# Kernel tuning notes

Hardware: AMD Instinct MI355X
Metric: run time of the kernel (lower is better)

Reference implementation:

```python
import jax, jax.numpy as jnp
import numpy as np
import math

B, S, D = 32, 2048, 1024


def setup_inputs() -> dict:
    key = jax.random.key(0)
    ks = jax.random.split(key, 8)
    x = jax.random.normal(ks[0], (B, S, D), dtype=jnp.float32)
    # right-padding mask: True = padding, each row has a random valid length in [S//2, S]
    lengths = jax.random.randint(ks[1], (B, 1), S // 2, S + 1)
    attention_mask = jnp.arange(S)[None, :] >= lengths  # [B, S] bool
    scale = 1.0 / math.sqrt(D)
    gate_w1 = jax.random.normal(ks[2], (D, D // 2), dtype=jnp.float32) * scale
    gate_b1 = jnp.zeros((D // 2,), dtype=jnp.float32)
    gate_w2 = jax.random.normal(ks[3], (D // 2, 1), dtype=jnp.float32) * scale
    gate_b2 = jnp.zeros((1,), dtype=jnp.float32)
    decay_lambda = jnp.float32(0.05)
    attention_query = jax.random.normal(ks[4], (D,), dtype=jnp.float32)
    key_w = jax.random.normal(ks[5], (D, D), dtype=jnp.float32) * scale
    key_b = jnp.zeros((D,), dtype=jnp.float32)
    return {
        "utterance_embeddings": x,
        "attention_mask": attention_mask,
        "gate_w1": gate_w1, "gate_b1": gate_b1,
        "gate_w2": gate_w2, "gate_b2": gate_b2,
        "decay_lambda": decay_lambda,
        "attention_query": attention_query,
        "key_w": key_w, "key_b": key_b,
    }


def reference(utterance_embeddings, attention_mask, gate_w1, gate_b1, gate_w2,
              gate_b2, decay_lambda, attention_query, key_w, key_b):
    x = utterance_embeddings  # [B, S, D]
    bsz, seq_len, dim = x.shape
    # suppression gate: Linear -> GELU(exact) -> Linear -> Sigmoid, output [B, S, 1]
    h = jax.nn.gelu(jnp.einsum('bsd,dk->bsk', x, gate_w1) + gate_b1, approximate=False)
    gate = jax.nn.sigmoid(jnp.einsum('bsk,ko->bso', h, gate_w2) + gate_b2)
    gated = x * gate  # [B, S, D]
    keys = jnp.einsum('bsd,de->bse', gated, key_w) + key_b  # [B, S, D]
    logits = jnp.einsum('d,bsd->bs', attention_query, keys) / jnp.sqrt(jnp.float32(dim))
    t_idx = jnp.arange(seq_len, dtype=jnp.float32)[None, :]  # [1, S]
    valid_lengths = jnp.sum(~attention_mask, axis=1, keepdims=True).astype(jnp.float32)
    penalty_idx = jnp.maximum(valid_lengths - 1.0 - t_idx, 0.0)  # [B, S]
    pos_lambda = jax.nn.softplus(decay_lambda)
    decayed = logits - pos_lambda * penalty_idx
    decayed = jnp.where(attention_mask, jnp.float32(-10000.0), decayed)
    alpha = jax.nn.softmax(decayed, axis=1)  # [B, S]
    scene_vector = jnp.einsum('bs,bsd->bd', alpha, gated)  # [B, D]
    return scene_vector
```

## Files before the change

kernel.cpp:

```cpp
#include <hip/hip_runtime.h>
#include <hip/hip_bf16.h>
#include <math.h>

#define BQ 32
#define SQ 2048
#define DQ 1024
#define NQ 512
#define MQ (BQ*SQ)
#define BM 64
#define BN 512
#define BK 32

typedef __attribute__((ext_vector_type(8))) short bf16x8;
typedef __attribute__((ext_vector_type(4))) short bf16x4;
typedef __attribute__((ext_vector_type(4))) float f32x4;

__device__ __forceinline__ short f2bf(float f){
  return __builtin_bit_cast(short, __float2bfloat16(f));
}

__device__ __forceinline__ void gload_lds16(const void* g, void* l){
  __builtin_amdgcn_global_load_lds(
      (const __attribute__((address_space(1))) unsigned int*)g,
      (__attribute__((address_space(3))) unsigned int*)l, 16, 0, 0);
}

__global__ void k_w1t(const float* __restrict__ w1, short* __restrict__ w1t){
  int i = blockIdx.x*256 + threadIdx.x;
  if (i >= NQ*DQ) return;
  int n = i >> 10, k = i & (DQ-1);
  w1t[i] = f2bf(w1[(size_t)k*NQ + n]);
}

__global__ void k_wq(const float* __restrict__ kw, const float* __restrict__ kb,
                     const float* __restrict__ q, float* __restrict__ wq){
  __shared__ float sh[4];
  int d = blockIdx.x, t = threadIdx.x;
  const float* row = (d < DQ) ? (kw + (size_t)d*DQ) : kb;
  float s = 0.f;
  for (int e=t;e<DQ;e+=256) s += row[e]*q[e];
  #pragma unroll
  for (int o=32;o;o>>=1) s += __shfl_down(s,o);
  if ((t&63)==0) sh[t>>6]=s;
  __syncthreads();
  if (t==0) wq[d] = sh[0]+sh[1]+sh[2]+sh[3];
}

__global__ void k_det(const unsigned int* __restrict__ m, int* __restrict__ flag){
  __shared__ int so, sf;
  int t = threadIdx.x;
  if (t==0){ so=0; sf=0; }
  __syncthreads();
  int o=0, f1=0;
  for (int i=t;i<MQ/4;i+=256){
    unsigned v = m[i];
    if (v==0x3F800000u) f1=1;
    else if (v>1u) o=1;
  }
  if (o) atomicOr(&so,1);
  if (f1) atomicOr(&sf,1);
  __syncthreads();
  if (t==0) *flag = so?2:(sf?1:0);
}

__global__ __launch_bounds__(256) void k_len(const void* __restrict__ maskp,
                                             const int* __restrict__ flag,
                                             int* __restrict__ lens){
  __shared__ int sh[4];
  int b = blockIdx.x, t = threadIdx.x;
  int fl = *flag;
  const unsigned char* m8 = (const unsigned char*)maskp;
  const float* mf = (const float*)maskp;
  const int* mi = (const int*)maskp;
  int cnt = 0;
  #pragma unroll
  for (int i=0;i<8;i++){
    size_t idx = (size_t)b*SQ + t + i*256;
    int mm = (fl==2) ? (m8[idx]!=0) : (fl==1) ? (mf[idx]!=0.0f) : (mi[idx]!=0);
    cnt += mm^1;
  }
  #pragma unroll
  for (int o=32;o;o>>=1) cnt += __shfl_down(cnt,o);
  if ((t&63)==0) sh[t>>6]=cnt;
  __syncthreads();
  if (t==0) lens[b] = sh[0]+sh[1]+sh[2]+sh[3];
}

__global__ __launch_bounds__(512) void k_gate(
    const float* __restrict__ x, const short* __restrict__ w1t,
    const float* __restrict__ wq, const float* __restrict__ w2,
    const float* __restrict__ b1, const float* __restrict__ b2p,
    const float* __restrict__ lamp,
    const void* __restrict__ maskp, const int* __restrict__ flag,
    const int* __restrict__ lens,
    float* __restrict__ part, float* __restrict__ wsum)
{
  __shared__ __align__(16) short As[2][BM*BK];
  __shared__ __align__(16) short Bs[2][BN*BK];
  __shared__ float wqs[DQ];
  __shared__ float red[8][BM];
  __shared__ float wrow[BM];
  __shared__ float xqrow[BM];

  int tid = threadIdx.x;
  int bm = blockIdx.x;
  int m0 = bm*BM;
  int batch = bm >> 5;
  int s0 = (bm & 31) * 64;
  int lane = tid & 63, wid = tid >> 6;
  int wn = wid;
  int lo = lane & 15, hi = lane >> 4;

  wqs[tid]     = wq[tid];
  wqs[tid+512] = wq[tid+512];

  int ar = tid >> 3, ac = (tid & 7) * 4;
  const float* asrc = x + (size_t)(m0 + ar)*DQ + ac;
  const short* bsrc = w1t + (size_t)(tid>>2)*DQ + (tid&3)*8;

  float w2v[4], b1v[4];
  #pragma unroll
  for (int fn=0;fn<4;fn++){
    int n = wn*64 + fn*16 + lo;
    w2v[fn] = w2[n]; b1v[fn] = b1[n];
  }

  f32x4 r0 = *(const f32x4*)(asrc);
  #pragma unroll
  for (int i=0;i<4;i++)
    gload_lds16(bsrc + (size_t)i*128*DQ, &Bs[0][i*4096 + tid*8]);
  __syncthreads();
  float xqacc = 0.f;
  {
    f32x4 w0 = *(const f32x4*)(wqs + ac);
    #pragma unroll
    for (int j=0;j<4;j++) xqacc += r0[j]*w0[j];
    bf16x4 s0v;
    #pragma unroll
    for (int j=0;j<4;j++) s0v[j]=f2bf(r0[j]);
    *(bf16x4*)(&As[0][ar*BK + ac]) = s0v;
  }
  __syncthreads();

  f32x4 acc[4][4];
  #pragma unroll
  for (int a=0;a<4;a++)
    #pragma unroll
    for (int b=0;b<4;b++) acc[a][b] = (f32x4){0.f,0.f,0.f,0.f};

  for (int t=0;t<32;t++){
    int cur = t & 1, nxt = cur ^ 1;
    int k0n = (t+1)*BK;
    if (t < 31){
      r0 = *(const f32x4*)(asrc + k0n);
      #pragma unroll
      for (int i=0;i<4;i++)
        gload_lds16(bsrc + (size_t)i*128*DQ + k0n, &Bs[nxt][i*4096 + tid*8]);
    }
    bf16x8 af[4], bfr[4];
    #pragma unroll
    for (int fm=0;fm<4;fm++)
      af[fm] = *(const bf16x8*)(&As[cur][(fm*16+lo)*BK + hi*8]);
    #pragma unroll
    for (int fn=0;fn<4;fn++)
      bfr[fn] = *(const bf16x8*)(&Bs[cur][(wn*64+fn*16+lo)*BK + hi*8]);
    #pragma unroll
    for (int fm=0;fm<4;fm++)
      #pragma unroll
      for (int fn=0;fn<4;fn++)
        acc[fm][fn] = __builtin_amdgcn_mfma_f32_16x16x32_bf16(af[fm], bfr[fn], acc[fm][fn], 0,0,0);
    if (t < 31){
      f32x4 w0 = *(const f32x4*)(wqs + k0n + ac);
      #pragma unroll
      for (int j=0;j<4;j++) xqacc += r0[j]*w0[j];
      bf16x4 s0v;
      #pragma unroll
      for (int j=0;j<4;j++) s0v[j]=f2bf(r0[j]);
      *(bf16x4*)(&As[nxt][ar*BK + ac]) = s0v;
    }
    __syncthreads();
  }

  {
    float s = xqacc;
    s += __shfl_xor(s,1); s += __shfl_xor(s,2); s += __shfl_xor(s,4);
    if ((tid & 7) == 0) xqrow[ar] = s;
  }

  #pragma unroll
  for (int fm=0;fm<4;fm++){
    #pragma unroll
    for (int j=0;j<4;j++){
      float s = 0.f;
      #pragma unroll
      for (int fn=0;fn<4;fn++){
        float h = acc[fm][fn][j] + b1v[fn];
        float g = 0.5f*h*(1.0f + erff(h*0.70710678118f));
        s += g*w2v[fn];
      }
      s += __shfl_xor(s,1); s += __shfl_xor(s,2);
      s += __shfl_xor(s,4); s += __shfl_xor(s,8);
      if (lo == 0) red[wid][fm*16 + hi*4 + j] = s;
    }
  }
  __syncthreads();

  if (tid < 64){
    int s = s0 + tid;
    float gsum = b2p[0];
    #pragma unroll
    for (int w=0;w<8;w++) gsum += red[w][tid];
    float gate = 1.0f/(1.0f+expf(-gsum));
    float qb = wq[DQ];
    float lg = (gate*xqrow[tid] + qb)*0.03125f;
    float lam = lamp[0];
    float posl = fmaxf(lam,0.f) + log1pf(expf(-fabsf(lam)));
    int L = lens[batch];
    float pen = fmaxf((float)L - 1.0f - (float)s, 0.0f);
    int fl = *flag;
    size_t mi_ = (size_t)batch*SQ + s;
    int mm = (fl==2) ? (((const unsigned char*)maskp)[mi_]!=0)
           : (fl==1) ? (((const float*)maskp)[mi_]!=0.0f)
                     : (((const int*)maskp)[mi_]!=0);
    float e = mm ? 0.0f : expf(lg - posl*pen);
    wrow[tid] = e*gate;
    float tsum = e;
    #pragma unroll
    for (int o=1;o<64;o<<=1) tsum += __shfl_xor(tsum,o);
    if (tid==0) wsum[bm] = tsum;
  }
  __syncthreads();

  {
    int d0 = tid*2;
    const float* xb = x + (size_t)m0*DQ + d0;
    float a0=0.f, a1=0.f;
    #pragma unroll 8
    for (int s=0;s<64;s++){
      float w = wrow[s];
      float2 v = *(const float2*)(xb + (size_t)s*DQ);
      a0 += w*v.x; a1 += w*v.y;
    }
    *(float2*)(part + (size_t)bm*DQ + d0) = make_float2(a0,a1);
  }
}

__global__ __launch_bounds__(256) void k_fin(const float* __restrict__ part,
                                             const float* __restrict__ wsum,
                                             float* __restrict__ out){
  int i = blockIdx.x*256 + threadIdx.x;
  int b = i >> 10, d = i & 1023;
  float den = 0.f;
  #pragma unroll
  for (int c=0;c<32;c++) den += wsum[b*32+c];
  float s = 0.f;
  #pragma unroll
  for (int c=0;c<32;c++) s += part[((size_t)(b*32+c))*DQ + d];
  out[i] = s/den;
}

extern "C" void kernel_launch(void* const* d_in, const int* in_sizes, int n_in,
                              void* d_out, int out_size, void* d_ws, size_t ws_size,
                              hipStream_t stream)
{
  const float* x    = (const float*)d_in[0];
  const void*  mask = d_in[1];
  const float* w1   = (const float*)d_in[2];
  const float* b1   = (const float*)d_in[3];
  const float* w2   = (const float*)d_in[4];
  const float* b2   = (const float*)d_in[5];
  const float* lam  = (const float*)d_in[6];
  const float* q    = (const float*)d_in[7];
  const float* kw   = (const float*)d_in[8];
  const float* kb   = (const float*)d_in[9];
  char* ws = (char*)d_ws;
  short* w1t = (short*)ws;
  float* wq  = (float*)(ws + (1<<20));
  int* flag  = (int*)(ws + (1<<20) + 8192);
  int* lens  = (int*)(ws + (1<<20) + 8448);
  float* wsum= (float*)(ws + (1<<20) + 12544);
  float* part= (float*)(ws + (1<<20) + 20736);
  float* out = (float*)d_out;

  k_w1t<<<dim3((NQ*DQ+255)/256), 256, 0, stream>>>(w1, w1t);
  k_wq<<<dim3(DQ+1), 256, 0, stream>>>(kw, kb, q, wq);
  k_det<<<dim3(1), 256, 0, stream>>>((const unsigned int*)mask, flag);
  k_len<<<dim3(BQ), 256, 0, stream>>>(mask, flag, lens);
  k_gate<<<dim3(MQ/BM), 512, 0, stream>>>(x, w1t, wq, w2, b1, b2, lam,
                                          mask, flag, lens, part, wsum);
  k_fin<<<dim3((BQ*DQ)/256), 256, 0, stream>>>(part, wsum, out);
}
```

Before: 185.3 us.

## Split gate GEMM K-step into four barrier phases with fine-grained vmcnt waits

Restructures the gate GEMM main loop into four phases per K-tile. Each phase issues one quarter of the next B tile's direct-to-LDS loads, waits on a precise vmcnt, and runs four MFMAs at raised priority. The A operand is prefetched two tiles ahead, and the B row mapping is permuted so each phase loads exactly the 16 columns it consumes. It also adds a min-blocks-per-CU launch bound. The aim is to overlap global-to-LDS transfers with MFMA work at finer granularity and replace full syncthreads with raw barriers, at the cost of hand-counted waitcnts that are fragile and of more barriers per K-step.

```diff
diff --git a/kernel.cpp b/kernel.cpp
--- a/kernel.cpp
+++ b/kernel.cpp
@@ -14,6 +14,10 @@
 typedef __attribute__((ext_vector_type(8))) short bf16x8;
 typedef __attribute__((ext_vector_type(4))) short bf16x4;
 typedef __attribute__((ext_vector_type(4))) float f32x4;
+
+#define WAITVM(n) asm volatile("s_waitcnt vmcnt(" #n ")")
+#define WAITLG    asm volatile("s_waitcnt lgkmcnt(0)")
+#define SB0       __builtin_amdgcn_sched_barrier(0)
 
 __device__ __forceinline__ short f2bf(float f){
   return __builtin_bit_cast(short, __float2bfloat16(f));
@@ -86,7 +90,7 @@
   if (t==0) lens[b] = sh[0]+sh[1]+sh[2]+sh[3];
 }
 
-__global__ __launch_bounds__(512) void k_gate(
+__global__ __launch_bounds__(512, 4) void k_gate(
     const float* __restrict__ x, const short* __restrict__ w1t,
     const float* __restrict__ wq, const float* __restrict__ w2,
     const float* __restrict__ b1, const float* __restrict__ b2p,
@@ -106,7 +110,7 @@
   int bm = blockIdx.x;
   int m0 = bm*BM;
   int batch = bm >> 5;
-  int s0 = (bm & 31) * 64;
+  int sBase = (bm & 31) * 64;
   int lane = tid & 63, wid = tid >> 6;
   int wn = wid;
   int lo = lane & 15, hi = lane >> 4;
@@ -116,7 +120,15 @@
 
   int ar = tid >> 3, ac = (tid & 7) * 4;
   const float* asrc = x + (size_t)(m0 + ar)*DQ + ac;
-  const short* bsrc = w1t + (size_t)(tid>>2)*DQ + (tid&3)*8;
+  int br = tid >> 2;
+  int base_n = ((br >> 4) << 6) | (br & 15);
+  const short* bsrc0 = w1t + (size_t)base_n*DQ + (tid&3)*8;
+
+  int boff  = (wn*16 + lo)*BK + hi*8;
+  int aoff0 = (0*16 + lo)*BK + hi*8;
+  int aoff1 = (1*16 + lo)*BK + hi*8;
+  int aoff2 = (2*16 + lo)*BK + hi*8;
+  int aoff3 = (3*16 + lo)*BK + hi*8;
 
   float w2v[4], b1v[4];
   #pragma unroll
@@ -125,22 +137,24 @@
     w2v[fn] = w2[n]; b1v[fn] = b1[n];
   }
 
-  f32x4 r0 = *(const f32x4*)(asrc);
-  #pragma unroll
-  for (int i=0;i<4;i++)
-    gload_lds16(bsrc + (size_t)i*128*DQ, &Bs[0][i*4096 + tid*8]);
-  __syncthreads();
+  __syncthreads();
+
   float xqacc = 0.f;
+  f32x4 rA1, rA2 = (f32x4){0.f,0.f,0.f,0.f};
   {
+    f32x4 rA0 = *(const f32x4*)(asrc);
+    gload_lds16(bsrc0,          &Bs[0][0*4096 + tid*8]);
+    gload_lds16(bsrc0 + 16*DQ,  &Bs[0][1*4096 + tid*8]);
+    gload_lds16(bsrc0 + 32*DQ,  &Bs[0][2*4096 + tid*8]);
+    rA1 = *(const f32x4*)(asrc + BK);
+    gload_lds16(bsrc0 + 48*DQ,  &Bs[0][3*4096 + tid*8]);
     f32x4 w0 = *(const f32x4*)(wqs + ac);
-    #pragma unroll
-    for (int j=0;j<4;j++) xqacc += r0[j]*w0[j];
-    bf16x4 s0v;
-    #pragma unroll
-    for (int j=0;j<4;j++) s0v[j]=f2bf(r0[j]);
-    *(bf16x4*)(&As[0][ar*BK + ac]) = s0v;
-  }
-  __syncthreads();
+    xqacc += rA0[0]*w0[0] + rA0[1]*w0[1] + rA0[2]*w0[2] + rA0[3]*w0[3];
+    bf16x4 sv;
+    sv[0]=f2bf(rA0[0]); sv[1]=f2bf(rA0[1]); sv[2]=f2bf(rA0[2]); sv[3]=f2bf(rA0[3]);
+    *(bf16x4*)(&As[0][ar*BK + ac]) = sv;
+    WAITLG; SB0;
+  }
 
   f32x4 acc[4][4];
   #pragma unroll
@@ -148,38 +162,66 @@
     #pragma unroll
     for (int b=0;b<4;b++) acc[a][b] = (f32x4){0.f,0.f,0.f,0.f};
 
-  for (int t=0;t<32;t++){
-    int cur = t & 1, nxt = cur ^ 1;
-    int k0n = (t+1)*BK;
-    if (t < 31){
-      r0 = *(const f32x4*)(asrc + k0n);
-      #pragma unroll
-      for (int i=0;i<4;i++)
-        gload_lds16(bsrc + (size_t)i*128*DQ + k0n, &Bs[nxt][i*4096 + tid*8]);
+  bf16x8 af[4];
+
+#define PHASE_CORE(qq) do{                                                      \
+    __builtin_amdgcn_s_barrier(); SB0;                                          \
+    bf16x8 _b = *(const bf16x8*)(&Bs[cur][(qq)*4096 + boff]);                   \
+    if ((qq)==0){                                                               \
+      af[0] = *(const bf16x8*)(&As[cur][aoff0]);                                \
+      af[1] = *(const bf16x8*)(&As[cur][aoff1]);                                \
+      af[2] = *(const bf16x8*)(&As[cur][aoff2]);                                \
+      af[3] = *(const bf16x8*)(&As[cur][aoff3]);                                \
+    }                                                                           \
+    WAITLG; SB0;                                                                \
+    __builtin_amdgcn_s_setprio(1);                                              \
+    acc[0][qq] = __builtin_amdgcn_mfma_f32_16x16x32_bf16(af[0], _b, acc[0][qq],0,0,0); \
+    acc[1][qq] = __builtin_amdgcn_mfma_f32_16x16x32_bf16(af[1], _b, acc[1][qq],0,0,0); \
+    acc[2][qq] = __builtin_amdgcn_mfma_f32_16x16x32_bf16(af[2], _b, acc[2][qq],0,0,0); \
+    acc[3][qq] = __builtin_amdgcn_mfma_f32_16x16x32_bf16(af[3], _b, acc[3][qq],0,0,0); \
+    __builtin_amdgcn_s_setprio(0);                                              \
+  }while(0)
+
+  for (int t=0; t<31; ++t){
+    int cur = t&1, nxt = cur^1;
+    int kn = (t+1)*BK;
+    const short* bK = bsrc0 + kn;
+    short* BsN = &Bs[nxt][0];
+    gload_lds16(bK,           BsN + 0*4096 + tid*8);
+    SB0; WAITVM(5); SB0;
+    PHASE_CORE(0);
+    gload_lds16(bK + 16*DQ,   BsN + 1*4096 + tid*8);
+    SB0; WAITVM(5); SB0;
+    PHASE_CORE(1);
+    gload_lds16(bK + 32*DQ,   BsN + 2*4096 + tid*8);
+    if (t < 30){
+      rA2 = *(const f32x4*)(asrc + (t+2)*BK);
+      SB0; WAITVM(6); SB0;
+    } else {
+      SB0; WAITVM(5); SB0;
     }
-    bf16x8 af[4], bfr[4];
-    #pragma unroll
-    for (int fm=0;fm<4;fm++)
-      af[fm] = *(const bf16x8*)(&As[cur][(fm*16+lo)*BK + hi*8]);
-    #pragma unroll
-    for (int fn=0;fn<4;fn++)
-      bfr[fn] = *(const bf16x8*)(&Bs[cur][(wn*64+fn*16+lo)*BK + hi*8]);
-    #pragma unroll
-    for (int fm=0;fm<4;fm++)
-      #pragma unroll
-      for (int fn=0;fn<4;fn++)
-        acc[fm][fn] = __builtin_amdgcn_mfma_f32_16x16x32_bf16(af[fm], bfr[fn], acc[fm][fn], 0,0,0);
-    if (t < 31){
-      f32x4 w0 = *(const f32x4*)(wqs + k0n + ac);
-      #pragma unroll
-      for (int j=0;j<4;j++) xqacc += r0[j]*w0[j];
-      bf16x4 s0v;
-      #pragma unroll
-      for (int j=0;j<4;j++) s0v[j]=f2bf(r0[j]);
-      *(bf16x4*)(&As[nxt][ar*BK + ac]) = s0v;
+    PHASE_CORE(2);
+    gload_lds16(bK + 48*DQ,   BsN + 3*4096 + tid*8);
+    if (t < 30){ SB0; WAITVM(5); SB0; } else { SB0; WAITVM(4); SB0; }
+    PHASE_CORE(3);
+    {
+      f32x4 w0 = *(const f32x4*)(wqs + kn + ac);
+      xqacc += rA1[0]*w0[0] + rA1[1]*w0[1] + rA1[2]*w0[2] + rA1[3]*w0[3];
+      bf16x4 sv;
+      sv[0]=f2bf(rA1[0]); sv[1]=f2bf(rA1[1]); sv[2]=f2bf(rA1[2]); sv[3]=f2bf(rA1[3]);
+      *(bf16x4*)(&As[nxt][ar*BK + ac]) = sv;
+      WAITLG; SB0;
+      rA1 = rA2;
     }
-    __syncthreads();
-  }
+  }
+  {
+    int cur = 1;
+    SB0; WAITVM(3); SB0; PHASE_CORE(0);
+    SB0; WAITVM(2); SB0; PHASE_CORE(1);
+    SB0; WAITVM(1); SB0; PHASE_CORE(2);
+    SB0; WAITVM(0); SB0; PHASE_CORE(3);
+  }
+#undef PHASE_CORE
 
   {
     float s = xqacc;
@@ -206,7 +248,7 @@
   __syncthreads();
 
   if (tid < 64){
-    int s = s0 + tid;
+    int s = sBase + tid;
     float gsum = b2p[0];
     #pragma unroll
     for (int w=0;w<8;w++) gsum += red[w][tid];
```

Measured after the change: 184.8 us. Within noise of the previous version (-0.3%).

## Pre-convert x to bf16 in a separate pass and stream A tile via direct LDS loads

Applied to the files above, without the earlier changes.

Adds a k_xprep kernel that converts x to bf16 and computes the per-row x·wq dot product. The gate GEMM can then load its A tiles with global_load_lds, dropping the per-iteration fp32 register loads, conversions and the xq accumulation from the main loop. The new kernel also requests higher occupancy through launch bounds. In exchange there is an extra full pass over x (read 256MB, write 128MB of bf16) plus a 128MB workspace requirement, with the old kernel kept as a fallback when the workspace is too small.

```diff
diff --git a/kernel.cpp b/kernel.cpp
--- a/kernel.cpp
+++ b/kernel.cpp
@@ -44,6 +44,32 @@
   if ((t&63)==0) sh[t>>6]=s;
   __syncthreads();
   if (t==0) wq[d] = sh[0]+sh[1]+sh[2]+sh[3];
+}
+
+__global__ __launch_bounds__(256) void k_xprep(
+    const float* __restrict__ x, const float* __restrict__ wq,
+    short* __restrict__ xbf, float* __restrict__ xqv)
+{
+  __shared__ float sh[4];
+  int t = threadIdx.x;
+  int r = blockIdx.x*2 + (t>>7);
+  int seg = (t & 127) * 8;
+  const float* xr = x + (size_t)r*DQ + seg;
+  f32x4 a = *(const f32x4*)(xr);
+  f32x4 b = *(const f32x4*)(xr + 4);
+  f32x4 wa = *(const f32x4*)(wq + seg);
+  f32x4 wb = *(const f32x4*)(wq + seg + 4);
+  float s = a[0]*wa[0]+a[1]*wa[1]+a[2]*wa[2]+a[3]*wa[3]
+          + b[0]*wb[0]+b[1]*wb[1]+b[2]*wb[2]+b[3]*wb[3];
+  bf16x8 sv;
+  #pragma unroll
+  for (int j=0;j<4;j++){ sv[j]=f2bf(a[j]); sv[4+j]=f2bf(b[j]); }
+  *(bf16x8*)(xbf + (size_t)r*DQ + seg) = sv;
+  #pragma unroll
+  for (int o=1;o<64;o<<=1) s += __shfl_xor(s,o);
+  if ((t&63)==0) sh[t>>6]=s;
+  __syncthreads();
+  if ((t&127)==0) xqv[r] = sh[(t>>7)*2] + sh[(t>>7)*2+1];
 }
 
 __global__ void k_det(const unsigned int* __restrict__ m, int* __restrict__ flag){
@@ -86,107 +112,17 @@
   if (t==0) lens[b] = sh[0]+sh[1]+sh[2]+sh[3];
 }
 
-__global__ __launch_bounds__(512) void k_gate(
-    const float* __restrict__ x, const short* __restrict__ w1t,
-    const float* __restrict__ wq, const float* __restrict__ w2,
-    const float* __restrict__ b1, const float* __restrict__ b2p,
-    const float* __restrict__ lamp,
+__device__ __forceinline__ void gate_epilogue(
+    int tid, int wid, int lo, int hi, int bm, int m0, int batch, int sBase,
+    const f32x4 acc[4][4], const float* w2v, const float* b1v,
+    float (*red)[BM], float* wrow,
+    const float* __restrict__ xqv, const float* __restrict__ wq,
+    const float* __restrict__ b2p, const float* __restrict__ lamp,
     const void* __restrict__ maskp, const int* __restrict__ flag,
     const int* __restrict__ lens,
-    float* __restrict__ part, float* __restrict__ wsum)
+    const float* __restrict__ x, float* __restrict__ part,
+    float* __restrict__ wsum)
 {
-  __shared__ __align__(16) short As[2][BM*BK];
-  __shared__ __align__(16) short Bs[2][BN*BK];
-  __shared__ float wqs[DQ];
-  __shared__ float red[8][BM];
-  __shared__ float wrow[BM];
-  __shared__ float xqrow[BM];
-
-  int tid = threadIdx.x;
-  int bm = blockIdx.x;
-  int m0 = bm*BM;
-  int batch = bm >> 5;
-  int s0 = (bm & 31) * 64;
-  int lane = tid & 63, wid = tid >> 6;
-  int wn = wid;
-  int lo = lane & 15, hi = lane >> 4;
-
-  wqs[tid]     = wq[tid];
-  wqs[tid+512] = wq[tid+512];
-
-  int ar = tid >> 3, ac = (tid & 7) * 4;
-  const float* asrc = x + (size_t)(m0 + ar)*DQ + ac;
-  const short* bsrc = w1t + (size_t)(tid>>2)*DQ + (tid&3)*8;
-
-  float w2v[4], b1v[4];
-  #pragma unroll
-  for (int fn=0;fn<4;fn++){
-    int n = wn*64 + fn*16 + lo;
-    w2v[fn] = w2[n]; b1v[fn] = b1[n];
-  }
-
-  f32x4 r0 = *(const f32x4*)(asrc);
-  #pragma unroll
-  for (int i=0;i<4;i++)
-    gload_lds16(bsrc + (size_t)i*128*DQ, &Bs[0][i*4096 + tid*8]);
-  __syncthreads();
-  float xqacc = 0.f;
-  {
-    f32x4 w0 = *(const f32x4*)(wqs + ac);
-    #pragma unroll
-    for (int j=0;j<4;j++) xqacc += r0[j]*w0[j];
-    bf16x4 s0v;
-    #pragma unroll
-    for (int j=0;j<4;j++) s0v[j]=f2bf(r0[j]);
-    *(bf16x4*)(&As[0][ar*BK + ac]) = s0v;
-  }
-  __syncthreads();
-
-  f32x4 acc[4][4];
-  #pragma unroll
-  for (int a=0;a<4;a++)
-    #pragma unroll
-    for (int b=0;b<4;b++) acc[a][b] = (f32x4){0.f,0.f,0.f,0.f};
-
-  for (int t=0;t<32;t++){
-    int cur = t & 1, nxt = cur ^ 1;
-    int k0n = (t+1)*BK;
-    if (t < 31){
-      r0 = *(const f32x4*)(asrc + k0n);
-      #pragma unroll
-      for (int i=0;i<4;i++)
-        gload_lds16(bsrc + (size_t)i*128*DQ + k0n, &Bs[nxt][i*4096 + tid*8]);
-    }
-    bf16x8 af[4], bfr[4];
-    #pragma unroll
-    for (int fm=0;fm<4;fm++)
-      af[fm] = *(const bf16x8*)(&As[cur][(fm*16+lo)*BK + hi*8]);
-    #pragma unroll
-    for (int fn=0;fn<4;fn++)
-      bfr[fn] = *(const bf16x8*)(&Bs[cur][(wn*64+fn*16+lo)*BK + hi*8]);
-    #pragma unroll
-    for (int fm=0;fm<4;fm++)
-      #pragma unroll
-      for (int fn=0;fn<4;fn++)
-        acc[fm][fn] = __builtin_amdgcn_mfma_f32_16x16x32_bf16(af[fm], bfr[fn], acc[fm][fn], 0,0,0);
-    if (t < 31){
-      f32x4 w0 = *(const f32x4*)(wqs + k0n + ac);
-      #pragma unroll
-      for (int j=0;j<4;j++) xqacc += r0[j]*w0[j];
-      bf16x4 s0v;
-      #pragma unroll
-      for (int j=0;j<4;j++) s0v[j]=f2bf(r0[j]);
-      *(bf16x4*)(&As[nxt][ar*BK + ac]) = s0v;
-    }
-    __syncthreads();
-  }
-
-  {
-    float s = xqacc;
-    s += __shfl_xor(s,1); s += __shfl_xor(s,2); s += __shfl_xor(s,4);
-    if ((tid & 7) == 0) xqrow[ar] = s;
-  }
-
   #pragma unroll
   for (int fm=0;fm<4;fm++){
     #pragma unroll
@@ -206,13 +142,13 @@
   __syncthreads();
 
   if (tid < 64){
-    int s = s0 + tid;
+    int s = sBase + tid;
     float gsum = b2p[0];
     #pragma unroll
     for (int w=0;w<8;w++) gsum += red[w][tid];
     float gate = 1.0f/(1.0f+expf(-gsum));
     float qb = wq[DQ];
-    float lg = (gate*xqrow[tid] + qb)*0.03125f;
+    float lg = (gate*xqv[m0 + tid] + qb)*0.03125f;
     float lam = lamp[0];
     float posl = fmaxf(lam,0.f) + log1pf(expf(-fabsf(lam)));
     int L = lens[batch];
@@ -243,6 +179,187 @@
     }
     *(float2*)(part + (size_t)bm*DQ + d0) = make_float2(a0,a1);
   }
+}
+
+__global__ __launch_bounds__(512, 4) void k_gate_lean(
+    const short* __restrict__ xbf, const float* __restrict__ x,
+    const short* __restrict__ w1t, const float* __restrict__ xqv,
+    const float* __restrict__ wq, const float* __restrict__ w2,
+    const float* __restrict__ b1, const float* __restrict__ b2p,
+    const float* __restrict__ lamp,
+    const void* __restrict__ maskp, const int* __restrict__ flag,
+    const int* __restrict__ lens,
+    float* __restrict__ part, float* __restrict__ wsum)
+{
+  __shared__ __align__(16) short As[2][BM*BK];
+  __shared__ __align__(16) short Bs[2][BN*BK];
+  __shared__ float red[8][BM];
+  __shared__ float wrow[BM];
+
+  int tid = threadIdx.x;
+  int bm = blockIdx.x;
+  int m0 = bm*BM;
+  int batch = bm >> 5;
+  int sBase = (bm & 31) * 64;
+  int lane = tid & 63, wid = tid >> 6;
+  int wn = wid;
+  int lo = lane & 15, hi = lane >> 4;
+
+  const short* bsrc = w1t + (size_t)(tid>>2)*DQ + (tid&3)*8;
+  const short* asrc = xbf + (size_t)(m0 + (tid>>2))*DQ + (tid&3)*8;
+
+  float w2v[4], b1v[4];
+  #pragma unroll
+  for (int fn=0;fn<4;fn++){
+    int n = wn*64 + fn*16 + lo;
+    w2v[fn] = w2[n]; b1v[fn] = b1[n];
+  }
+
+  #pragma unroll
+  for (int i=0;i<4;i++)
+    gload_lds16(bsrc + (size_t)i*128*DQ, &Bs[0][i*4096 + tid*8]);
+  if (tid < 256) gload_lds16(asrc, &As[0][tid*8]);
+  __syncthreads();
+
+  f32x4 acc[4][4];
+  #pragma unroll
+  for (int a=0;a<4;a++)
+    #pragma unroll
+    for (int b=0;b<4;b++) acc[a][b] = (f32x4){0.f,0.f,0.f,0.f};
+
+  for (int t=0;t<32;t++){
+    int cur = t & 1, nxt = cur ^ 1;
+    int kn = (t+1)*BK;
+    if (t < 31){
+      #pragma unroll
+      for (int i=0;i<4;i++)
+        gload_lds16(bsrc + (size_t)i*128*DQ + kn, &Bs[nxt][i*4096 + tid*8]);
+      if (tid < 256) gload_lds16(asrc + kn, &As[nxt][tid*8]);
+    }
+    bf16x8 af[4], bfr[4];
+    #pragma unroll
+    for (int fm=0;fm<4;fm++)
+      af[fm] = *(const bf16x8*)(&As[cur][(fm*16+lo)*BK + hi*8]);
+    #pragma unroll
+    for (int fn=0;fn<4;fn++)
+      bfr[fn] = *(const bf16x8*)(&Bs[cur][(wn*64+fn*16+lo)*BK + hi*8]);
+    #pragma unroll
+    for (int fm=0;fm<4;fm++)
+      #pragma unroll
+      for (int fn=0;fn<4;fn++)
+        acc[fm][fn] = __builtin_amdgcn_mfma_f32_16x16x32_bf16(af[fm], bfr[fn], acc[fm][fn], 0,0,0);
+    __syncthreads();
+  }
+
+  gate_epilogue(tid, wid, lo, hi, bm, m0, batch, sBase, acc, w2v, b1v,
+                red, wrow, xqv, wq, b2p, lamp, maskp, flag, lens,
+                x, part, wsum);
+}
+
+__global__ __launch_bounds__(512) void k_gate_fb(
+    const float* __restrict__ x, const short* __restrict__ w1t,
+    const float* __restrict__ wq, const float* __restrict__ w2,
+    const float* __restrict__ b1, const float* __restrict__ b2p,
+    const float* __restrict__ lamp,
+    const void* __restrict__ maskp, const int* __restrict__ flag,
+    const int* __restrict__ lens,
+    float* __restrict__ part, float* __restrict__ wsum, float* __restrict__ xqv)
+{
+  __shared__ __align__(16) short As[2][BM*BK];
+  __shared__ __align__(16) short Bs[2][BN*BK];
+  __shared__ float wqs[DQ];
+  __shared__ float red[8][BM];
+  __shared__ float wrow[BM];
+
+  int tid = threadIdx.x;
+  int bm = blockIdx.x;
+  int m0 = bm*BM;
+  int batch = bm >> 5;
+  int sBase = (bm & 31) * 64;
+  int lane = tid & 63, wid = tid >> 6;
+  int wn = wid;
+  int lo = lane & 15, hi = lane >> 4;
+
+  wqs[tid] = wq[tid];
+  if (tid < 512) wqs[tid+512] = wq[tid+512];
+
+  int ar = tid >> 3, ac = (tid & 7) * 4;
+  const float* asrc = x + (size_t)(m0 + ar)*DQ + ac;
+  const short* bsrc = w1t + (size_t)(tid>>2)*DQ + (tid&3)*8;
+
+  float w2v[4], b1v[4];
+  #pragma unroll
+  for (int fn=0;fn<4;fn++){
+    int n = wn*64 + fn*16 + lo;
+    w2v[fn] = w2[n]; b1v[fn] = b1[n];
+  }
+
+  f32x4 r0 = *(const f32x4*)(asrc);
+  #pragma unroll
+  for (int i=0;i<4;i++)
+    gload_lds16(bsrc + (size_t)i*128*DQ, &Bs[0][i*4096 + tid*8]);
+  __syncthreads();
+  float xqacc = 0.f;
+  {
+    f32x4 w0 = *(const f32x4*)(wqs + ac);
+    #pragma unroll
+    for (int j=0;j<4;j++) xqacc += r0[j]*w0[j];
+    bf16x4 s0v;
+    #pragma unroll
+    for (int j=0;j<4;j++) s0v[j]=f2bf(r0[j]);
+    *(bf16x4*)(&As[0][ar*BK + ac]) = s0v;
+  }
+  __syncthreads();
+
+  f32x4 acc[4][4];
+  #pragma unroll
+  for (int a=0;a<4;a++)
+    #pragma unroll
+    for (int b=0;b<4;b++) acc[a][b] = (f32x4){0.f,0.f,0.f,0.f};
+
+  for (int t=0;t<32;t++){
+    int cur = t & 1, nxt = cur ^ 1;
+    int kn = (t+1)*BK;
+    if (t < 31){
+      r0 = *(const f32x4*)(asrc + kn);
+      #pragma unroll
+      for (int i=0;i<4;i++)
+        gload_lds16(bsrc + (size_t)i*128*DQ + kn, &Bs[nxt][i*4096 + tid*8]);
+    }
+    bf16x8 af[4], bfr[4];
+    #pragma unroll
+    for (int fm=0;fm<4;fm++)
+      af[fm] = *(const bf16x8*)(&As[cur][(fm*16+lo)*BK + hi*8]);
+    #pragma unroll
+    for (int fn=0;fn<4;fn++)
+      bfr[fn] = *(const bf16x8*)(&Bs[cur][(wn*64+fn*16+lo)*BK + hi*8]);
+    #pragma unroll
+    for (int fm=0;fm<4;fm++)
+      #pragma unroll
+      for (int fn=0;fn<4;fn++)
+        acc[fm][fn] = __builtin_amdgcn_mfma_f32_16x16x32_bf16(af[fm], bfr[fn], acc[fm][fn], 0,0,0);
+    if (t < 31){
+      f32x4 w0 = *(const f32x4*)(wqs + kn + ac);
+      #pragma unroll
+      for (int j=0;j<4;j++) xqacc += r0[j]*w0[j];
+      bf16x4 s0v;
+      #pragma unroll
+      for (int j=0;j<4;j++) s0v[j]=f2bf(r0[j]);
+      *(bf16x4*)(&As[nxt][ar*BK + ac]) = s0v;
+    }
+    __syncthreads();
+  }
+
+  {
+    float s = xqacc;
+    s += __shfl_xor(s,1); s += __shfl_xor(s,2); s += __shfl_xor(s,4);
+    if ((tid & 7) == 0) xqv[m0 + ar] = s;
+  }
+  __syncthreads();
+
+  gate_epilogue(tid, wid, lo, hi, bm, m0, batch, sBase, acc, w2v, b1v,
+                red, wrow, xqv, wq, b2p, lamp, maskp, flag, lens,
+                x, part, wsum);
 }
 
 __global__ __launch_bounds__(256) void k_fin(const float* __restrict__ part,
@@ -279,14 +396,26 @@
   int* flag  = (int*)(ws + (1<<20) + 8192);
   int* lens  = (int*)(ws + (1<<20) + 8448);
   float* wsum= (float*)(ws + (1<<20) + 12544);
-  float* part= (float*)(ws + (1<<20) + 20736);
+  float* xqv = (float*)(ws + (1<<20) + 32768);
+  float* part= (float*)(ws + (2<<20));
+  short* xbf = (short*)(ws + (8ull<<20));
   float* out = (float*)d_out;
+
+  const size_t NEEDED = (8ull<<20) + ((size_t)MQ*DQ*2);
 
   k_w1t<<<dim3((NQ*DQ+255)/256), 256, 0, stream>>>(w1, w1t);
   k_wq<<<dim3(DQ+1), 256, 0, stream>>>(kw, kb, q, wq);
   k_det<<<dim3(1), 256, 0, stream>>>((const unsigned int*)mask, flag);
   k_len<<<dim3(BQ), 256, 0, stream>>>(mask, flag, lens);
-  k_gate<<<dim3(MQ/BM), 512, 0, stream>>>(x, w1t, wq, w2, b1, b2, lam,
-                                          mask, flag, lens, part, wsum);
+
+  if (ws_size >= NEEDED){
+    k_xprep<<<dim3(MQ/2), 256, 0, stream>>>(x, wq, xbf, xqv);
+    k_gate_lean<<<dim3(MQ/BM), 512, 0, stream>>>(xbf, x, w1t, xqv, wq, w2,
+                                                 b1, b2, lam, mask, flag, lens,
+                                                 part, wsum);
+  } else {
+    k_gate_fb<<<dim3(MQ/BM), 512, 0, stream>>>(x, w1t, wq, w2, b1, b2, lam,
+                                               mask, flag, lens, part, wsum, xqv);
+  }
   k_fin<<<dim3((BQ*DQ)/256), 256, 0, stream>>>(part, wsum, out);
 }
```

Result: slower. 292.4 us (+57.8%).

## Retile gate GEMM to 128x256 with triple-buffered B and split pooling kernel

Applied to the files above, without the earlier changes.

The gate GEMM now uses 128x256 tiles, with the N dimension split across two blocks and the block index swizzled for cache locality. B is triple-buffered through direct-to-LDS loads, and the per-iteration __syncthreads is replaced by a waitcnt plus s_barrier with sched_barriers. Softmax weighting and pooling move into a separate k_wpool kernel that reads partial gate sums from workspace and covers 256 rows per block. The aim is better MFMA utilization and more overlap of loads with compute. The cost is an extra kernel launch and a second full read of x, since x is no longer pooled while its tile is resident.

```diff
diff --git a/kernel.cpp b/kernel.cpp
--- a/kernel.cpp
+++ b/kernel.cpp
@@ -7,13 +7,14 @@
 #define DQ 1024
 #define NQ 512
 #define MQ (BQ*SQ)
-#define BM 64
-#define BN 512
+#define BM 128
+#define BN 256
 #define BK 32
 
 typedef __attribute__((ext_vector_type(8))) short bf16x8;
-typedef __attribute__((ext_vector_type(4))) short bf16x4;
 typedef __attribute__((ext_vector_type(4))) float f32x4;
+
+#define SB0 __builtin_amdgcn_sched_barrier(0)
 
 __device__ __forceinline__ short f2bf(float f){
   return __builtin_bit_cast(short, __float2bfloat16(f));
@@ -89,58 +90,60 @@
 __global__ __launch_bounds__(512) void k_gate(
     const float* __restrict__ x, const short* __restrict__ w1t,
     const float* __restrict__ wq, const float* __restrict__ w2,
-    const float* __restrict__ b1, const float* __restrict__ b2p,
-    const float* __restrict__ lamp,
-    const void* __restrict__ maskp, const int* __restrict__ flag,
-    const int* __restrict__ lens,
-    float* __restrict__ part, float* __restrict__ wsum)
+    const float* __restrict__ b1,
+    float* __restrict__ gpart, float* __restrict__ xqv)
 {
   __shared__ __align__(16) short As[2][BM*BK];
-  __shared__ __align__(16) short Bs[2][BN*BK];
+  __shared__ __align__(16) short Bs[3][BN*BK];
   __shared__ float wqs[DQ];
-  __shared__ float red[8][BM];
-  __shared__ float wrow[BM];
-  __shared__ float xqrow[BM];
+  __shared__ float red[4][BM];
 
   int tid = threadIdx.x;
-  int bm = blockIdx.x;
-  int m0 = bm*BM;
-  int batch = bm >> 5;
-  int s0 = (bm & 31) * 64;
+  int phys = blockIdx.x;
+  int bid = ((phys & 7) << 7) | (phys >> 3);
+  int bm = bid >> 1, bn = bid & 1;
+  int m0 = bm*BM, n0 = bn*BN;
   int lane = tid & 63, wid = tid >> 6;
-  int wn = wid;
+  int wm = wid >> 2, wn = wid & 3;
   int lo = lane & 15, hi = lane >> 4;
 
   wqs[tid]     = wq[tid];
   wqs[tid+512] = wq[tid+512];
 
-  int ar = tid >> 3, ac = (tid & 7) * 4;
-  const float* asrc = x + (size_t)(m0 + ar)*DQ + ac;
-  const short* bsrc = w1t + (size_t)(tid>>2)*DQ + (tid&3)*8;
+  int ar = tid >> 2, acf = (tid & 3) * 8;
+  const float* asrc = x + (size_t)(m0 + ar)*DQ + acf;
+  const short* bsrc = w1t + (size_t)(n0 + (tid>>2))*DQ + (tid&3)*8;
 
   float w2v[4], b1v[4];
   #pragma unroll
   for (int fn=0;fn<4;fn++){
-    int n = wn*64 + fn*16 + lo;
+    int n = n0 + wn*64 + fn*16 + lo;
     w2v[fn] = w2[n]; b1v[fn] = b1[n];
   }
 
-  f32x4 r0 = *(const f32x4*)(asrc);
-  #pragma unroll
-  for (int i=0;i<4;i++)
-    gload_lds16(bsrc + (size_t)i*128*DQ, &Bs[0][i*4096 + tid*8]);
-  __syncthreads();
+  gload_lds16(bsrc,                       &Bs[0][tid*8]);
+  gload_lds16(bsrc + (size_t)128*DQ,      &Bs[0][4096 + tid*8]);
+  gload_lds16(bsrc + BK,                  &Bs[1][tid*8]);
+  gload_lds16(bsrc + (size_t)128*DQ + BK, &Bs[1][4096 + tid*8]);
+  f32x4 a0 = *(const f32x4*)(asrc);
+  f32x4 a1 = *(const f32x4*)(asrc + 4);
+  {
+    bf16x8 sv;
+    #pragma unroll
+    for (int j=0;j<4;j++){ sv[j]=f2bf(a0[j]); sv[4+j]=f2bf(a1[j]); }
+    *(bf16x8*)(&As[0][ar*BK + acf]) = sv;
+  }
+  asm volatile("s_waitcnt lgkmcnt(0)" ::: "memory");
+  SB0;
+  __builtin_amdgcn_s_barrier();
+  SB0;
   float xqacc = 0.f;
-  {
-    f32x4 w0 = *(const f32x4*)(wqs + ac);
-    #pragma unroll
-    for (int j=0;j<4;j++) xqacc += r0[j]*w0[j];
-    bf16x4 s0v;
-    #pragma unroll
-    for (int j=0;j<4;j++) s0v[j]=f2bf(r0[j]);
-    *(bf16x4*)(&As[0][ar*BK + ac]) = s0v;
-  }
-  __syncthreads();
+  if (bn == 0){
+    f32x4 w0 = *(const f32x4*)(wqs + acf);
+    f32x4 w1f = *(const f32x4*)(wqs + acf + 4);
+    #pragma unroll
+    for (int j=0;j<4;j++) xqacc += a0[j]*w0[j] + a1[j]*w1f[j];
+  }
 
   f32x4 acc[4][4];
   #pragma unroll
@@ -148,43 +151,59 @@
     #pragma unroll
     for (int b=0;b<4;b++) acc[a][b] = (f32x4){0.f,0.f,0.f,0.f};
 
-  for (int t=0;t<32;t++){
-    int cur = t & 1, nxt = cur ^ 1;
-    int k0n = (t+1)*BK;
+  f32x4 na0, na1;
+  for (int t=0; t<32; ++t){
+    int curA = t & 1;
+    int curB = t % 3;
     if (t < 31){
-      r0 = *(const f32x4*)(asrc + k0n);
-      #pragma unroll
-      for (int i=0;i<4;i++)
-        gload_lds16(bsrc + (size_t)i*128*DQ + k0n, &Bs[nxt][i*4096 + tid*8]);
-    }
+      na0 = *(const f32x4*)(asrc + (t+1)*BK);
+      na1 = *(const f32x4*)(asrc + (t+1)*BK + 4);
+    }
+    SB0;
+    if (t < 30){
+      int nb = (t+2) % 3;
+      const short* bk = bsrc + (t+2)*BK;
+      gload_lds16(bk,                  &Bs[nb][tid*8]);
+      gload_lds16(bk + (size_t)128*DQ, &Bs[nb][4096 + tid*8]);
+    }
+    SB0;
     bf16x8 af[4], bfr[4];
     #pragma unroll
     for (int fm=0;fm<4;fm++)
-      af[fm] = *(const bf16x8*)(&As[cur][(fm*16+lo)*BK + hi*8]);
-    #pragma unroll
-    for (int fn=0;fn<4;fn++)
-      bfr[fn] = *(const bf16x8*)(&Bs[cur][(wn*64+fn*16+lo)*BK + hi*8]);
+      af[fm] = *(const bf16x8*)(&As[curA][(wm*64+fm*16+lo)*BK + hi*8]);
+    #pragma unroll
+    for (int fn=0;fn<4;fn++){
+      int r = wn*64 + fn*16 + lo;
+      bfr[fn] = *(const bf16x8*)(&Bs[curB][(r>>7)*4096 + (r&127)*32 + hi*8]);
+    }
     #pragma unroll
     for (int fm=0;fm<4;fm++)
       #pragma unroll
       for (int fn=0;fn<4;fn++)
         acc[fm][fn] = __builtin_amdgcn_mfma_f32_16x16x32_bf16(af[fm], bfr[fn], acc[fm][fn], 0,0,0);
+    SB0;
     if (t < 31){
-      f32x4 w0 = *(const f32x4*)(wqs + k0n + ac);
+      if (bn == 0){
+        f32x4 w0 = *(const f32x4*)(wqs + (t+1)*BK + acf);
+        f32x4 w1f = *(const f32x4*)(wqs + (t+1)*BK + acf + 4);
+        #pragma unroll
+        for (int j=0;j<4;j++) xqacc += na0[j]*w0[j] + na1[j]*w1f[j];
+      }
+      bf16x8 sv;
       #pragma unroll
-      for (int j=0;j<4;j++) xqacc += r0[j]*w0[j];
-      bf16x4 s0v;
-      #pragma unroll
-      for (int j=0;j<4;j++) s0v[j]=f2bf(r0[j]);
-      *(bf16x4*)(&As[nxt][ar*BK + ac]) = s0v;
-    }
-    __syncthreads();
-  }
-
-  {
+      for (int j=0;j<4;j++){ sv[j]=f2bf(na0[j]); sv[4+j]=f2bf(na1[j]); }
+      *(bf16x8*)(&As[curA^1][ar*BK + acf]) = sv;
+    }
+    asm volatile("s_waitcnt lgkmcnt(0)" ::: "memory");
+    SB0;
+    __builtin_amdgcn_s_barrier();
+    SB0;
+  }
+
+  if (bn == 0){
     float s = xqacc;
-    s += __shfl_xor(s,1); s += __shfl_xor(s,2); s += __shfl_xor(s,4);
-    if ((tid & 7) == 0) xqrow[ar] = s;
+    s += __shfl_xor(s,1); s += __shfl_xor(s,2);
+    if ((tid & 3) == 0) xqv[m0 + ar] = s;
   }
 
   #pragma unroll
@@ -200,22 +219,40 @@
       }
       s += __shfl_xor(s,1); s += __shfl_xor(s,2);
       s += __shfl_xor(s,4); s += __shfl_xor(s,8);
-      if (lo == 0) red[wid][fm*16 + hi*4 + j] = s;
-    }
-  }
-  __syncthreads();
-
-  if (tid < 64){
-    int s = s0 + tid;
-    float gsum = b2p[0];
-    #pragma unroll
-    for (int w=0;w<8;w++) gsum += red[w][tid];
+      if (lo == 0) red[wn][wm*64 + fm*16 + hi*4 + j] = s;
+    }
+  }
+  __syncthreads();
+  if (tid < BM){
+    float g = red[0][tid] + red[1][tid] + red[2][tid] + red[3][tid];
+    gpart[(size_t)bn*MQ + m0 + tid] = g;
+  }
+}
+
+__global__ __launch_bounds__(256) void k_wpool(
+    const float* __restrict__ x, const float* __restrict__ gpart,
+    const float* __restrict__ xqv, const float* __restrict__ wq,
+    const float* __restrict__ b2p, const float* __restrict__ lamp,
+    const void* __restrict__ maskp, const int* __restrict__ flag,
+    const int* __restrict__ lens,
+    float* __restrict__ part, float* __restrict__ wsumv)
+{
+  __shared__ float wrow[256];
+  __shared__ float ssum[4];
+  int blk = blockIdx.x, t = threadIdx.x;
+  int batch = blk >> 3;
+  int sBase = (blk & 7) * 256;
+  size_t R0 = (size_t)blk * 256;
+  {
+    size_t r = R0 + t;
+    float gsum = b2p[0] + gpart[r] + gpart[(size_t)MQ + r];
     float gate = 1.0f/(1.0f+expf(-gsum));
     float qb = wq[DQ];
-    float lg = (gate*xqrow[tid] + qb)*0.03125f;
+    float lg = (gate*xqv[r] + qb)*0.03125f;
     float lam = lamp[0];
     float posl = fmaxf(lam,0.f) + log1pf(expf(-fabsf(lam)));
     int L = lens[batch];
+    int s = sBase + t;
     float pen = fmaxf((float)L - 1.0f - (float)s, 0.0f);
     int fl = *flag;
     size_t mi_ = (size_t)batch*SQ + s;
@@ -223,39 +260,38 @@
            : (fl==1) ? (((const float*)maskp)[mi_]!=0.0f)
                      : (((const int*)maskp)[mi_]!=0);
     float e = mm ? 0.0f : expf(lg - posl*pen);
-    wrow[tid] = e*gate;
-    float tsum = e;
-    #pragma unroll
-    for (int o=1;o<64;o<<=1) tsum += __shfl_xor(tsum,o);
-    if (tid==0) wsum[bm] = tsum;
-  }
-  __syncthreads();
-
-  {
-    int d0 = tid*2;
-    const float* xb = x + (size_t)m0*DQ + d0;
-    float a0=0.f, a1=0.f;
-    #pragma unroll 8
-    for (int s=0;s<64;s++){
-      float w = wrow[s];
-      float2 v = *(const float2*)(xb + (size_t)s*DQ);
-      a0 += w*v.x; a1 += w*v.y;
-    }
-    *(float2*)(part + (size_t)bm*DQ + d0) = make_float2(a0,a1);
-  }
+    wrow[t] = e*gate;
+    float ts = e;
+    #pragma unroll
+    for (int o=1;o<64;o<<=1) ts += __shfl_xor(ts,o);
+    if ((t&63)==0) ssum[t>>6] = ts;
+  }
+  __syncthreads();
+  if (t==0) wsumv[blk] = ssum[0]+ssum[1]+ssum[2]+ssum[3];
+
+  int d0 = t*4;
+  const float* xb = x + R0*DQ + d0;
+  f32x4 a = {0.f,0.f,0.f,0.f};
+  #pragma unroll 8
+  for (int s=0;s<256;s++){
+    float w = wrow[s];
+    f32x4 v = *(const f32x4*)(xb + (size_t)s*DQ);
+    a[0] += w*v[0]; a[1] += w*v[1]; a[2] += w*v[2]; a[3] += w*v[3];
+  }
+  *(f32x4*)(part + (size_t)blk*DQ + d0) = a;
 }
 
 __global__ __launch_bounds__(256) void k_fin(const float* __restrict__ part,
-                                             const float* __restrict__ wsum,
+                                             const float* __restrict__ wsumv,
                                              float* __restrict__ out){
   int i = blockIdx.x*256 + threadIdx.x;
   int b = i >> 10, d = i & 1023;
   float den = 0.f;
   #pragma unroll
-  for (int c=0;c<32;c++) den += wsum[b*32+c];
+  for (int c=0;c<8;c++) den += wsumv[b*8+c];
   float s = 0.f;
   #pragma unroll
-  for (int c=0;c<32;c++) s += part[((size_t)(b*32+c))*DQ + d];
+  for (int c=0;c<8;c++) s += part[((size_t)(b*8+c))*DQ + d];
   out[i] = s/den;
 }
 
@@ -274,19 +310,23 @@
   const float* kw   = (const float*)d_in[8];
   const float* kb   = (const float*)d_in[9];
   char* ws = (char*)d_ws;
-  short* w1t = (short*)ws;
-  float* wq  = (float*)(ws + (1<<20));
-  int* flag  = (int*)(ws + (1<<20) + 8192);
-  int* lens  = (int*)(ws + (1<<20) + 8448);
-  float* wsum= (float*)(ws + (1<<20) + 12544);
-  float* part= (float*)(ws + (1<<20) + 20736);
-  float* out = (float*)d_out;
+  short* w1t   = (short*)ws;
+  float* wq    = (float*)(ws + (1<<20));
+  int*   flag  = (int*)(ws + (1<<20) + 8192);
+  int*   lens  = (int*)(ws + (1<<20) + 8448);
+  float* wsumv = (float*)(ws + (1<<20) + 12544);
+  float* xqv   = (float*)(ws + (1<<20) + 32768);
+  float* gpart = (float*)(ws + (2<<20));
+  float* part  = (float*)(ws + (3<<20));
+  float* out   = (float*)d_out;
 
   k_w1t<<<dim3((NQ*DQ+255)/256), 256, 0, stream>>>(w1, w1t);
   k_wq<<<dim3(DQ+1), 256, 0, stream>>>(kw, kb, q, wq);
   k_det<<<dim3(1), 256, 0, stream>>>((const unsigned int*)mask, flag);
   k_len<<<dim3(BQ), 256, 0, stream>>>(mask, flag, lens);
-  k_gate<<<dim3(MQ/BM), 512, 0, stream>>>(x, w1t, wq, w2, b1, b2, lam,
-                                          mask, flag, lens, part, wsum);
-  k_fin<<<dim3((BQ*DQ)/256), 256, 0, stream>>>(part, wsum, out);
-}
+  k_gate<<<dim3((MQ/BM)*(NQ/BN)), 512, 0, stream>>>(x, w1t, wq, w2, b1,
+                                                    gpart, xqv);
+  k_wpool<<<dim3(MQ/256), 256, 0, stream>>>(x, gpart, xqv, wq, b2, lam,
+                                            mask, flag, lens, part, wsumv);
+  k_fin<<<dim3((BQ*DQ)/256), 256, 0, stream>>>(part, wsumv, out);
+}
```

Measured after the change: 187.1 us. About the same (+1.0%).
